# Kernel tuning notes

Measured on AMD Instinct MI355X. Metric: run time of the kernel, lower is better.

The kernel has to match this reference:

```python
import jax, jax.numpy as jnp
import numpy as np

N, F_IN, H, P, R = 50000, 384, 128, 128, 16
E = 500000


def _lin_params(key, fan_in, fan_out):
    k1, k2 = jax.random.split(key)
    s = 1.0 / np.sqrt(fan_in)
    W = jax.random.uniform(k1, (fan_in, fan_out), jnp.float32, -s, s)
    b = jax.random.uniform(k2, (fan_out,), jnp.float32, -s, s)
    return W, b


def setup_inputs() -> dict:
    key = jax.random.key(0)
    ks = jax.random.split(key, 16)
    x = jax.random.normal(ks[0], (N, F_IN), jnp.float32)
    edge_index = jax.random.randint(ks[1], (2, E), 0, N, jnp.int64)
    W_gcn1, b_gcn1 = _lin_params(ks[2], F_IN, H)
    W_ti, b_ti = _lin_params(ks[3], F_IN, F_IN)      # CrossFusion.text_info (384 -> dim=384)
    W_gi, b_gi = _lin_params(ks[4], H, F_IN)          # CrossFusion.graph_info (128 -> 384)
    W_v, b_v = _lin_params(ks[5], F_IN, F_IN)         # CrossFusion.value
    Wl1, bl1 = _lin_params(ks[6], F_IN, F_IN // 2)    # left_generator hidden
    Wl2, bl2 = _lin_params(ks[7], F_IN // 2, P * R)
    Wr1, br1 = _lin_params(ks[8], F_IN, F_IN // 2)    # right_generator hidden
    Wr2, br2 = _lin_params(ks[9], F_IN // 2, R * F_IN)
    W_gcn2, b_gcn2 = _lin_params(ks[10], P, H)        # fusion_gcn (128 -> 128)
    W_gp, b_gp = _lin_params(ks[11], P, P)            # graph_proj
    return dict(x=x, edge_index=edge_index, W_gcn1=W_gcn1, b_gcn1=b_gcn1,
                W_ti=W_ti, b_ti=b_ti, W_gi=W_gi, b_gi=b_gi, W_v=W_v, b_v=b_v,
                Wl1=Wl1, bl1=bl1, Wl2=Wl2, bl2=bl2, Wr1=Wr1, br1=br1, Wr2=Wr2, br2=br2,
                W_gcn2=W_gcn2, b_gcn2=b_gcn2, W_gp=W_gp, b_gp=b_gp)


def _gcn(x, W, b, src, dst, n):
    # PyG GCNConv: self-loops + symmetric degree normalization, aggregate at dst.
    xw = x @ W
    loop = jnp.arange(n, dtype=src.dtype)
    s = jnp.concatenate([src, loop])
    d = jnp.concatenate([dst, loop])
    deg = jax.ops.segment_sum(jnp.ones_like(d, dtype=xw.dtype), d, num_segments=n)
    dinv = jnp.where(deg > 0, jax.lax.rsqrt(deg), 0.0)
    norm = dinv[s] * dinv[d]                           # [E+N]
    out = jax.ops.segment_sum(norm[:, None] * xw[s], d, num_segments=n)
    return out + b


def _cross_fusion(text_feat, graph_feat, row, col, W_ti, b_ti, W_gi, b_gi, W_v, b_v):
    n, dim = text_feat.shape[0], W_ti.shape[1]
    t_info = text_feat @ W_ti + b_ti                   # [N, dim]
    g_info = graph_feat @ W_gi + b_gi                  # [N, dim]
    v = text_feat @ W_v + b_v                          # [N, dim]
    scores = jnp.sum(t_info[row] * g_info[col], axis=-1) / np.sqrt(dim)   # [E]
    m = jax.ops.segment_max(scores, row, num_segments=n)                  # scatter_softmax
    e = jnp.exp(scores - m[row])
    denom = jax.ops.segment_sum(e, row, num_segments=n)
    attn = e / denom[row]
    out = jax.ops.segment_sum(attn[:, None] * v[col], row, num_segments=n)
    return out + text_feat


def _forward(x, edge_index, W_gcn1, b_gcn1, W_ti, b_ti, W_gi, b_gi, W_v, b_v,
             Wl1, bl1, Wl2, bl2, Wr1, br1, Wr2, br2, W_gcn2, b_gcn2, W_gp, b_gp):
    src, dst = edge_index[0], edge_index[1]
    n = x.shape[0]
    g_emb = _gcn(x, W_gcn1, b_gcn1, src, dst, n)
    x_fused = _cross_fusion(x, g_emb, src, dst, W_ti, b_ti, W_gi, b_gi, W_v, b_v)
    # N > 40000 -> low-rank chunked projection (chunking is pure batching; vectorize)
    left = (jax.nn.relu(x_fused @ Wl1 + bl1) @ Wl2 + bl2).reshape(n, P, R)
    right = (jax.nn.relu(x_fused @ Wr1 + br1) @ Wr2 + br2).reshape(n, R, F_IN)
    temp = jnp.einsum('nrf,nf->nr', right, x)
    p_t = jnp.einsum('npr,nr->np', left, temp)         # [N, P]
    g2 = _gcn(p_t, W_gcn2, b_gcn2, src, dst, n)        # dropout is identity in eval
    p_g = g2 @ W_gp + b_gp
    p_t = p_t / jnp.maximum(jnp.linalg.norm(p_t, axis=-1, keepdims=True), 1e-12)
    p_g = p_g / jnp.maximum(jnp.linalg.norm(p_g, axis=-1, keepdims=True), 1e-12)
    alignment = jnp.sum(p_t * p_g, axis=1)
    return alignment, p_t, p_g, g2


def reference(x, edge_index, W_gcn1, b_gcn1, W_ti, b_ti, W_gi, b_gi, W_v, b_v,
              Wl1, bl1, Wl2, bl2, Wr1, br1, Wr2, br2, W_gcn2, b_gcn2, W_gp, b_gp):
    return _forward(x, edge_index, W_gcn1, b_gcn1, W_ti, b_ti, W_gi, b_gi, W_v, b_v,
                    Wl1, bl1, Wl2, bl2, Wr1, br1, Wr2, br2, W_gcn2, b_gcn2, W_gp, b_gp)
```

## Files before the change

kernel.cpp:

```cpp
#include <hip/hip_runtime.h>

typedef unsigned int u32;
typedef unsigned short u16;
typedef short s16x8 __attribute__((ext_vector_type(8)));
typedef u16 u16x8 __attribute__((ext_vector_type(8)));
typedef float f32x4 __attribute__((ext_vector_type(4)));

#define FIN 384
#define HD  128
#define PD  128
#define RD  16

#define GLOAD16(g, l)                                                          \
  __builtin_amdgcn_global_load_lds(                                            \
      (const __attribute__((address_space(1))) void*)(g),                      \
      (__attribute__((address_space(3))) void*)(l), 16, 0, 0)

__device__ __forceinline__ u16 f2bf(float f) {
  u32 u = __float_as_uint(f);
  u32 r = (u + 0x7fffu + ((u >> 16) & 1u)) >> 16;
  return (u16)r;
}
__device__ __forceinline__ float bf2f(u16 h) {
  return __uint_as_float(((u32)h) << 16);
}

__device__ __forceinline__ int xcd_wgid() {
  int nwg = gridDim.x, orig = blockIdx.x;
  int q = nwg >> 3, r = nwg & 7, xcd = orig & 7, idx = orig >> 3;
  return (xcd < r ? xcd * (q + 1) : r * (q + 1) + (xcd - r) * q) + idx;
}

struct CvtEnt { const float* s; u16* d; int K, N, mode, blk0; };
struct CvtDesc { CvtEnt e[12]; int n; };

__global__ void cvt_all_k(CvtDesc dsc) {
  int b = blockIdx.x;
  int ei = 0;
  while (ei + 1 < dsc.n && dsc.e[ei + 1].blk0 <= b) ++ei;
  CvtEnt E = dsc.e[ei];
  int i = (b - E.blk0) * 256 + (int)threadIdx.x;
  int tot = E.K * E.N;
  if (i >= tot) return;
  float v;
  if (E.mode == 0) {
    int c = i / E.K, k = i - c * E.K;
    v = E.s[(size_t)k * E.N + c];
  } else if (E.mode == 1) {
    v = E.s[i];
  } else {
    int q = i / 384, f = i - q * 384;
    v = E.s[(size_t)(q >> 4) * 6144 + (q & 15) * 384 + f];
  }
  E.d[i] = f2bf(v);
}

__global__ void hist_k(const int* __restrict__ src, const int* __restrict__ dst,
                       u32* __restrict__ cnt, int n, int E) {
  int i = blockIdx.x * 256 + threadIdx.x;
  if (i < E) {
    atomicAdd(&cnt[src[i]], 1u);
    atomicAdd(&cnt[n + dst[i]], 1u);
  }
}

__global__ __launch_bounds__(1024)
void scanA_k(const u32* __restrict__ cnt, u32* __restrict__ off,
             u32* __restrict__ bsum, int n2) {
  __shared__ u32 sh[1024];
  int i = blockIdx.x * 1024 + (int)threadIdx.x;
  u32 v = (i < n2) ? cnt[i] : 0u;
  sh[threadIdx.x] = v;
  __syncthreads();
  for (int s = 1; s < 1024; s <<= 1) {
    u32 t = (threadIdx.x >= (u32)s) ? sh[threadIdx.x - s] : 0u;
    __syncthreads();
    sh[threadIdx.x] += t;
    __syncthreads();
  }
  if (i < n2) off[i] = sh[threadIdx.x] - v;
  if (threadIdx.x == 1023) bsum[blockIdx.x] = sh[1023];
}

__global__ void scanB_k(u32* __restrict__ bsum, int nb) {
  int l = threadIdx.x;
  u32 carry = 0u;
  for (int base = 0; base < nb; base += 64) {
    u32 v = (base + l < nb) ? bsum[base + l] : 0u;
    for (int s = 1; s < 64; s <<= 1) {
      u32 t = __shfl_up(v, s);
      if (l >= s) v += t;
    }
    if (base + l < nb) bsum[base + l] = v + carry;
    carry += __shfl(v, 63);
  }
}

__global__ __launch_bounds__(1024)
void scanC_k(u32* __restrict__ off, u32* __restrict__ cur,
             const u32* __restrict__ bsum, int n2) {
  int b = blockIdx.x;
  int i = b * 1024 + (int)threadIdx.x;
  if (i >= n2) return;
  u32 add = (b > 0) ? bsum[b - 1] : 0u;
  u32 o = off[i] + add;
  off[i] = o;
  cur[i] = o;
}

__global__ void fill_k(const int* __restrict__ src, const int* __restrict__ dst,
                       u32* __restrict__ cur, u32* __restrict__ adj, int n, int E) {
  int i = blockIdx.x * 256 + threadIdx.x;
  if (i >= E) return;
  int s = src[i], d = dst[i];
  u32 ps = atomicAdd(&cur[s], 1u);
  adj[ps] = (u32)d;
  u32 pd = atomicAdd(&cur[n + d], 1u);
  adj[pd] = (u32)s;
}

__global__ void dinv_k(const u32* __restrict__ cd, float* __restrict__ dinv, int n) {
  int i = blockIdx.x * 256 + threadIdx.x;
  if (i < n) dinv[i] = 1.0f / sqrtf((float)(cd[i] + 1u));
}

template <int WF32, int WBF>
__global__ void gcn_agg_k(const u16* __restrict__ xw, const float* __restrict__ dinv,
                          const u32* __restrict__ off, const u32* __restrict__ cnt,
                          const u32* __restrict__ nbr, const float* __restrict__ bias,
                          float* __restrict__ outf, u16* __restrict__ outb, int n) {
  int node = (blockIdx.x * blockDim.x + threadIdx.x) >> 6;
  int lane = threadIdx.x & 63;
  if (node >= n) return;
  float di = dinv[node];
  ushort2 v = ((const ushort2*)(xw + (size_t)node * HD))[lane];
  float ax = di * di * bf2f(v.x), ay = di * di * bf2f(v.y);
  u32 i = off[node], end = i + cnt[node];
  for (; i + 4 <= end; i += 4) {
    int s0 = (int)nbr[i],     s1 = (int)nbr[i + 1];
    int s2 = (int)nbr[i + 2], s3 = (int)nbr[i + 3];
    float w0 = di * dinv[s0], w1 = di * dinv[s1];
    float w2 = di * dinv[s2], w3 = di * dinv[s3];
    ushort2 u0 = ((const ushort2*)(xw + (size_t)s0 * HD))[lane];
    ushort2 u1 = ((const ushort2*)(xw + (size_t)s1 * HD))[lane];
    ushort2 u2 = ((const ushort2*)(xw + (size_t)s2 * HD))[lane];
    ushort2 u3 = ((const ushort2*)(xw + (size_t)s3 * HD))[lane];
    ax = fmaf(w0, bf2f(u0.x), ax); ay = fmaf(w0, bf2f(u0.y), ay);
    ax = fmaf(w1, bf2f(u1.x), ax); ay = fmaf(w1, bf2f(u1.y), ay);
    ax = fmaf(w2, bf2f(u2.x), ax); ay = fmaf(w2, bf2f(u2.y), ay);
    ax = fmaf(w3, bf2f(u3.x), ax); ay = fmaf(w3, bf2f(u3.y), ay);
  }
  for (; i < end; ++i) {
    int s0 = (int)nbr[i];
    float w0 = di * dinv[s0];
    ushort2 u0 = ((const ushort2*)(xw + (size_t)s0 * HD))[lane];
    ax = fmaf(w0, bf2f(u0.x), ax);
    ay = fmaf(w0, bf2f(u0.y), ay);
  }
  float2 b = ((const float2*)bias)[lane];
  ax += b.x; ay += b.y;
  if (WF32) ((float2*)(outf + (size_t)node * HD))[lane] = make_float2(ax, ay);
  if (WBF) {
    ushort2 ob; ob.x = f2bf(ax); ob.y = f2bf(ay);
    ((ushort2*)(outb + (size_t)node * HD))[lane] = ob;
  }
}

__global__ void attn_fused_k(const u32* __restrict__ off, const u32* __restrict__ cnt,
                             const u32* __restrict__ adj,
                             const u16* __restrict__ ti, int TS,
                             const u16* __restrict__ gi, int GS,
                             const u16* __restrict__ vmat, int VS,
                             const u16* __restrict__ xb,
                             float* __restrict__ scores,
                             u16* __restrict__ xf, int n) {
  int node = (blockIdx.x * blockDim.x + threadIdx.x) >> 6;
  int lane = threadIdx.x & 63;
  if (node >= n) return;
  u32 o = off[node], c = cnt[node];
  u32 end = o + c;
  float acc[6] = {0.f, 0.f, 0.f, 0.f, 0.f, 0.f};
  const float sc = 0.05103103630798288f;
  if (c > 0) {
    const u16* tp = ti + (size_t)node * TS;
    float tf[6];
#pragma unroll
    for (int q = 0; q < 3; ++q) {
      ushort2 tv = *(const ushort2*)(tp + q * 128 + lane * 2);
      tf[q * 2] = bf2f(tv.x);
      tf[q * 2 + 1] = bf2f(tv.y);
    }
    if (c <= 64) {
      float sreg = -1e30f;
      u32 i = o;
      for (; i + 2 <= end; i += 2) {
        int d0 = (int)adj[i], d1 = (int)adj[i + 1];
        const u16* g0 = gi + (size_t)d0 * GS;
        const u16* g1 = gi + (size_t)d1 * GS;
        float dot0 = 0.f, dot1 = 0.f;
#pragma unroll
        for (int q = 0; q < 3; ++q) {
          ushort2 a = *(const ushort2*)(g0 + q * 128 + lane * 2);
          ushort2 b = *(const ushort2*)(g1 + q * 128 + lane * 2);
          dot0 = fmaf(tf[q * 2], bf2f(a.x), dot0);
          dot0 = fmaf(tf[q * 2 + 1], bf2f(a.y), dot0);
          dot1 = fmaf(tf[q * 2], bf2f(b.x), dot1);
          dot1 = fmaf(tf[q * 2 + 1], bf2f(b.y), dot1);
        }
#pragma unroll
        for (int s2 = 32; s2 >= 1; s2 >>= 1) {
          dot0 += __shfl_xor(dot0, s2);
          dot1 += __shfl_xor(dot1, s2);
        }
        int idx = (int)(i - o);
        if (lane == idx) sreg = dot0 * sc;
        if (lane == idx + 1) sreg = dot1 * sc;
      }
      if (i < end) {
        int d0 = (int)adj[i];
        const u16* g0 = gi + (size_t)d0 * GS;
        float dot0 = 0.f;
#pragma unroll
        for (int q = 0; q < 3; ++q) {
          ushort2 a = *(const ushort2*)(g0 + q * 128 + lane * 2);
          dot0 = fmaf(tf[q * 2], bf2f(a.x), dot0);
          dot0 = fmaf(tf[q * 2 + 1], bf2f(a.y), dot0);
        }
#pragma unroll
        for (int s2 = 32; s2 >= 1; s2 >>= 1) dot0 += __shfl_xor(dot0, s2);
        if (lane == (int)(i - o)) sreg = dot0 * sc;
      }
      float mx = sreg;
#pragma unroll
      for (int s2 = 32; s2 >= 1; s2 >>= 1) mx = fmaxf(mx, __shfl_xor(mx, s2));
      float ew = (lane < (int)c) ? expf(sreg - mx) : 0.f;
      float den = ew;
#pragma unroll
      for (int s2 = 32; s2 >= 1; s2 >>= 1) den += __shfl_xor(den, s2);
      float wreg = ew / den;
      i = o;
      for (; i + 2 <= end; i += 2) {
        int d0 = (int)adj[i], d1 = (int)adj[i + 1];
        int idx = (int)(i - o);
        float w0 = __shfl(wreg, idx);
        float w1 = __shfl(wreg, idx + 1);
        const u16* v0 = vmat + (size_t)d0 * VS;
        const u16* v1 = vmat + (size_t)d1 * VS;
#pragma unroll
        for (int q = 0; q < 3; ++q) {
          ushort2 a = *(const ushort2*)(v0 + q * 128 + lane * 2);
          ushort2 b = *(const ushort2*)(v1 + q * 128 + lane * 2);
          acc[q * 2]     = fmaf(w0, bf2f(a.x), acc[q * 2]);
          acc[q * 2 + 1] = fmaf(w0, bf2f(a.y), acc[q * 2 + 1]);
          acc[q * 2]     = fmaf(w1, bf2f(b.x), acc[q * 2]);
          acc[q * 2 + 1] = fmaf(w1, bf2f(b.y), acc[q * 2 + 1]);
        }
      }
      if (i < end) {
        int d0 = (int)adj[i];
        float w0 = __shfl(wreg, (int)(i - o));
        const u16* v0 = vmat + (size_t)d0 * VS;
#pragma unroll
        for (int q = 0; q < 3; ++q) {
          ushort2 a = *(const ushort2*)(v0 + q * 128 + lane * 2);
          acc[q * 2]     = fmaf(w0, bf2f(a.x), acc[q * 2]);
          acc[q * 2 + 1] = fmaf(w0, bf2f(a.y), acc[q * 2 + 1]);
        }
      }
    } else {
      float mx = -1e30f;
      u32 i = o;
      for (; i < end; ++i) {
        int d0 = (int)adj[i];
        const u16* g0 = gi + (size_t)d0 * GS;
        float dot0 = 0.f;
#pragma unroll
        for (int q = 0; q < 3; ++q) {
          ushort2 a = *(const ushort2*)(g0 + q * 128 + lane * 2);
          dot0 = fmaf(tf[q * 2], bf2f(a.x), dot0);
          dot0 = fmaf(tf[q * 2 + 1], bf2f(a.y), dot0);
        }
#pragma unroll
        for (int s2 = 32; s2 >= 1; s2 >>= 1) dot0 += __shfl_xor(dot0, s2);
        dot0 *= sc;
        if (lane == 0) scores[i] = dot0;
        mx = fmaxf(mx, dot0);
      }
      float den = 0.f;
      for (u32 k = o + lane; k < end; k += 64) den += expf(scores[k] - mx);
#pragma unroll
      for (int s2 = 32; s2 >= 1; s2 >>= 1) den += __shfl_xor(den, s2);
      float invden = 1.0f / den;
      for (i = o; i < end; ++i) {
        int d0 = (int)adj[i];
        float w0 = expf(scores[i] - mx) * invden;
        const u16* v0 = vmat + (size_t)d0 * VS;
#pragma unroll
        for (int q = 0; q < 3; ++q) {
          ushort2 a = *(const ushort2*)(v0 + q * 128 + lane * 2);
          acc[q * 2]     = fmaf(w0, bf2f(a.x), acc[q * 2]);
          acc[q * 2 + 1] = fmaf(w0, bf2f(a.y), acc[q * 2 + 1]);
        }
      }
    }
  }
  const u16* xp = xb + (size_t)node * FIN;
  u16* op = xf + (size_t)node * FIN;
#pragma unroll
  for (int q = 0; q < 3; ++q) {
    ushort2 xv = *(const ushort2*)(xp + q * 128 + lane * 2);
    ushort2 ov;
    ov.x = f2bf(acc[q * 2] + bf2f(xv.x));
    ov.y = f2bf(acc[q * 2 + 1] + bf2f(xv.y));
    *(ushort2*)(op + q * 128 + lane * 2) = ov;
  }
}

template <int EPI, int OUTBF>
__global__ __launch_bounds__(256)
void mgemm_k(const u16* __restrict__ Abf, int As, const u16* __restrict__ WT,
             const float* __restrict__ bias, const float* __restrict__ bias_b, int bsplit,
             void* __restrict__ Cp, u16* __restrict__ Cbf2,
             float* __restrict__ tmp, int M, int K, int Nc, int ncx) {
  __shared__ u16 Albuf[2][128 * 32];
  __shared__ u16 Blbuf[2][128 * 32];
  const int t = threadIdx.x;
  const int lane = t & 63;
  const int wave = t >> 6;
  const int wr = wave >> 1, wc = wave & 1;
  const int wgid = xcd_wgid();
  const int ctile = wgid % ncx;
  const int row0 = (wgid / ncx) * 128;
  const int col0 = ctile * 128;
  const int sr = t >> 2;
  const int sk = (t & 3) * 8;
  const int nt = K >> 5;

  f32x4 acc[4][4] = {};

  auto stage = [&](int buf, int k0) {
#pragma unroll
    for (int h = 0; h < 2; ++h) {
      int ar = row0 + h * 64 + sr;
      if (ar >= M) ar = M - 1;
      GLOAD16(Abf + (size_t)ar * As + k0 + sk, &Albuf[buf][h * 2048 + wave * 512]);
    }
#pragma unroll
    for (int h = 0; h < 2; ++h) {
      int bc = col0 + h * 64 + sr;
      if (bc >= Nc) bc = Nc - 1;
      GLOAD16(WT + (size_t)bc * K + k0 + sk, &Blbuf[buf][h * 2048 + wave * 512]);
    }
  };

  stage(0, 0);
  int buf = 0;
  for (int tk = 0; tk < nt; ++tk) {
    __syncthreads();
    if (tk + 1 < nt) stage(buf ^ 1, (tk + 1) << 5);
    const u16* Al = Albuf[buf];
    const u16* Bl = Blbuf[buf];
    s16x8 a[4], b[4];
#pragma unroll
    for (int m = 0; m < 4; ++m)
      a[m] = *(const s16x8*)(Al + (wr * 64 + m * 16 + (lane & 15)) * 32 + (lane >> 4) * 8);
#pragma unroll
    for (int j = 0; j < 4; ++j)
      b[j] = *(const s16x8*)(Bl + (wc * 64 + j * 16 + (lane & 15)) * 32 + (lane >> 4) * 8);
#pragma unroll
    for (int mc = 0; mc < 4; ++mc)
#pragma unroll
      for (int jr = 0; jr < 4; ++jr)
        acc[mc][jr] = __builtin_amdgcn_mfma_f32_16x16x32_bf16(b[mc], a[jr], acc[mc][jr], 0, 0, 0);
    buf ^= 1;
  }

  if constexpr (EPI <= 2) {
#pragma unroll
    for (int jr = 0; jr < 4; ++jr) {
      int row = row0 + wr * 64 + jr * 16 + (lane & 15);
      if (row >= M) continue;
#pragma unroll
      for (int mc = 0; mc < 4; ++mc) {
        int colb = col0 + wc * 64 + mc * 16 + (lane >> 4) * 4;
        if (colb >= Nc) continue;
        float4 bv = make_float4(0.f, 0.f, 0.f, 0.f);
        if (EPI >= 1) {
          const float* bp = (colb < bsplit) ? bias + colb : bias_b + (colb - bsplit);
          bv = *(const float4*)bp;
        }
        float v0 = acc[mc][jr][0] + bv.x;
        float v1 = acc[mc][jr][1] + bv.y;
        float v2 = acc[mc][jr][2] + bv.z;
        float v3 = acc[mc][jr][3] + bv.w;
        if (EPI == 2) {
          v0 = fmaxf(v0, 0.f); v1 = fmaxf(v1, 0.f);
          v2 = fmaxf(v2, 0.f); v3 = fmaxf(v3, 0.f);
        }
        if (OUTBF) {
          ushort4 ov;
          ov.x = f2bf(v0); ov.y = f2bf(v1); ov.z = f2bf(v2); ov.w = f2bf(v3);
          *(ushort4*)((u16*)Cp + (size_t)row * Nc + colb) = ov;
        } else {
          *(float4*)((float*)Cp + (size_t)row * Nc + colb) = make_float4(v0, v1, v2, v3);
        }
      }
    }
  } else if constexpr (EPI == 6) {
#pragma unroll
    for (int jr = 0; jr < 4; ++jr) {
      int row = row0 + wr * 64 + jr * 16 + (lane & 15);
      if (row >= M) continue;
#pragma unroll
      for (int mc = 0; mc < 4; ++mc) {
        int colb = col0 + wc * 64 + mc * 16 + (lane >> 4) * 4;
        if (colb < 2 * FIN) {
          const float* bp = (colb < bsplit) ? bias + colb : bias_b + (colb - bsplit);
          float4 bv = *(const float4*)bp;
          ushort4 ov;
          ov.x = f2bf(acc[mc][jr][0] + bv.x);
          ov.y = f2bf(acc[mc][jr][1] + bv.y);
          ov.z = f2bf(acc[mc][jr][2] + bv.z);
          ov.w = f2bf(acc[mc][jr][3] + bv.w);
          *(ushort4*)((u16*)Cp + (size_t)row * (2 * FIN) + colb) = ov;
        } else {
          int c2 = colb - 2 * FIN;
          ushort4 ov;
          ov.x = f2bf(acc[mc][jr][0]);
          ov.y = f2bf(acc[mc][jr][1]);
          ov.z = f2bf(acc[mc][jr][2]);
          ov.w = f2bf(acc[mc][jr][3]);
          *(ushort4*)(Cbf2 + (size_t)row * HD + c2) = ov;
        }
      }
    }
  } else {
    u16* slice = (u16*)Cp + (size_t)ctile * M * 8;
    float4 b4[4];
#pragma unroll
    for (int mc = 0; mc < 4; ++mc)
      b4[mc] = *(const float4*)&bias[col0 + wc * 64 + mc * 16 + (lane >> 4) * 4];
#pragma unroll
    for (int jr = 0; jr < 4; ++jr) {
      int row = row0 + wr * 64 + jr * 16 + (lane & 15);
      int rc = row < M ? row : M - 1;
      float4 tv = *(const float4*)&tmp[(size_t)rc * RD + (lane >> 4) * 4];
      ushort4 outp;
#pragma unroll
      for (int mc = 0; mc < 4; ++mc) {
        float s = (acc[mc][jr][0] + b4[mc].x) * tv.x +
                  (acc[mc][jr][1] + b4[mc].y) * tv.y +
                  (acc[mc][jr][2] + b4[mc].z) * tv.z +
                  (acc[mc][jr][3] + b4[mc].w) * tv.w;
        s += __shfl_xor(s, 16);
        s += __shfl_xor(s, 32);
        ((u16*)&outp)[mc] = f2bf(s);
      }
      if (lane < 16 && row < M)
        *(ushort4*)(slice + (size_t)row * 8 + wc * 4) = outp;
    }
  }
}

__global__ void ptgather_k(const u16* __restrict__ ptP, float* __restrict__ pt,
                           u16* __restrict__ ptb, int n) {
  int g = blockIdx.x * 256 + threadIdx.x;
  if (g >= n * 16) return;
  int row = g >> 4, ct = g & 15;
  const u16* sp = ptP + ((size_t)ct * n + (size_t)row) * 8;
  ushort4 a = ((const ushort4*)sp)[0];
  ushort4 b = ((const ushort4*)sp)[1];
  float* dp = pt + (size_t)row * PD + ct * 8;
  ((float4*)dp)[0] = make_float4(bf2f(a.x), bf2f(a.y), bf2f(a.z), bf2f(a.w));
  ((float4*)dp)[1] = make_float4(bf2f(b.x), bf2f(b.y), bf2f(b.z), bf2f(b.w));
  u16* db = ptb + (size_t)row * PD + ct * 8;
  ((ushort4*)db)[0] = a;
  ((ushort4*)db)[1] = b;
}

#define VM6  asm volatile("s_waitcnt vmcnt(6)" ::: "memory")
#define VM0  asm volatile("s_waitcnt vmcnt(0)" ::: "memory")
#define VMNOP
#define BARR asm volatile("s_barrier" ::: "memory")

__global__ __launch_bounds__(512)
void ygemm8_k(const u16* __restrict__ X, const u16* __restrict__ QT,
              const u16* __restrict__ Ar, float* __restrict__ tmpP, int M) {
  __shared__ u16 Al[2][16384];
  __shared__ u16 Bl[2][16384];
  const int t = threadIdx.x;
  const int lane = t & 63;
  const int wave = t >> 6;
  const int wr = wave >> 2;
  const int wcn = wave & 3;
  const int wgid = xcd_wgid();
  const int ctile = wgid % 12;
  const int row0 = (wgid / 12) * 256;
  const int col0 = ctile * 256;

  const int srow = t >> 3;
  const int sgk  = (((t & 7) ^ (srow & 7)) << 3);
  const int sdst = t * 8;

  const int pc0 = (((lane >> 4)) ^ (lane & 7)) << 3;
  const int pc1 = ((((lane >> 4) + 4)) ^ (lane & 7)) << 3;
  const int arow = (wr * 128 + (lane & 15)) << 6;
  const int brow = (wcn * 64 + (lane & 15)) << 6;

  f32x4 acc[8][4] = {};
  s16x8 a[4][2], b[4][2];

#define STGA8(bf, h, kt) do {                                                  \
    int r0_ = row0 + (h) * 128 + srow;                                         \
    int r1_ = r0_ + 64;                                                        \
    if (r0_ >= M) r0_ = M - 1;                                                 \
    if (r1_ >= M) r1_ = M - 1;                                                 \
    GLOAD16(X + (size_t)r0_ * 384 + (kt) * 64 + sgk, &Al[bf][(h) * 8192 + sdst]);        \
    GLOAD16(X + (size_t)r1_ * 384 + (kt) * 64 + sgk, &Al[bf][(h) * 8192 + 4096 + sdst]); \
  } while (0)

#define STGB8(bf, h, kt) do {                                                  \
    int c0_ = col0 + (h) * 128 + srow;                                         \
    GLOAD16(QT + (size_t)c0_ * 384 + (kt) * 64 + sgk, &Bl[bf][(h) * 8192 + sdst]);       \
    GLOAD16(QT + (size_t)(c0_ + 64) * 384 + (kt) * 64 + sgk,                   \
            &Bl[bf][(h) * 8192 + 4096 + sdst]);                                \
  } while (0)

#define LDA8(bf, mh) do {                                                      \
    _Pragma("unroll") for (int m2_ = 0; m2_ < 4; ++m2_) {                      \
      const u16* p_ = &Al[bf][arow + ((mh) * 4 + m2_) * 1024];                 \
      a[m2_][0] = *(const s16x8*)(p_ + pc0);                                   \
      a[m2_][1] = *(const s16x8*)(p_ + pc1);                                   \
    }                                                                          \
  } while (0)

#define LDB8(bf, jh) do {                                                      \
    _Pragma("unroll") for (int j2_ = 0; j2_ < 2; ++j2_) {                      \
      const u16* p_ = &Bl[bf][brow + ((jh) * 2 + j2_) * 1024];                 \
      b[(jh) * 2 + j2_][0] = *(const s16x8*)(p_ + pc0);                        \
      b[(jh) * 2 + j2_][1] = *(const s16x8*)(p_ + pc1);                        \
    }                                                                          \
  } while (0)

#define MQ8(mh, jh) do {                                                       \
    __builtin_amdgcn_s_setprio(1);                                             \
    _Pragma("unroll") for (int m2_ = 0; m2_ < 4; ++m2_)                        \
      _Pragma("unroll") for (int j2_ = 0; j2_ < 2; ++j2_)                      \
        _Pragma("unroll") for (int ks_ = 0; ks_ < 2; ++ks_)                    \
          acc[(mh) * 4 + m2_][(jh) * 2 + j2_] =                                \
              __builtin_amdgcn_mfma_f32_16x16x32_bf16(                         \
                  a[m2_][ks_], b[(jh) * 2 + j2_][ks_],                         \
                  acc[(mh) * 4 + m2_][(jh) * 2 + j2_], 0, 0, 0);               \
    __builtin_amdgcn_s_setprio(0);                                             \
  } while (0)

  STGA8(0, 0, 0); STGA8(0, 1, 0); STGB8(0, 0, 0); STGB8(0, 1, 0);
  STGA8(1, 0, 1); STGB8(1, 0, 1); STGB8(1, 1, 1);
  VM6; BARR;

#define ITER8(i, VMP3, VMP7, DOSTG)                                                          \
   LDA8(0,0); LDB8(0,0); STGA8(1,1,2*(i)+1);                   BARR; MQ8(0,0); BARR;  \
   LDB8(0,1);                                                  BARR; MQ8(0,1); BARR;  \
   LDA8(0,1); if (DOSTG) STGB8(0,0,2*(i)+2);                   BARR; MQ8(1,0); BARR;  \
   if (DOSTG) { STGB8(0,1,2*(i)+2); STGA8(0,0,2*(i)+2); } VMP3; BARR; MQ8(1,1); BARR; \
   LDA8(1,0); LDB8(1,0); if (DOSTG) STGA8(0,1,2*(i)+2);        BARR; MQ8(0,0); BARR;  \
   LDB8(1,1);                                                  BARR; MQ8(0,1); BARR;  \
   LDA8(1,1); if (DOSTG) STGB8(1,0,2*(i)+3);                   BARR; MQ8(1,0); BARR;  \
   if (DOSTG) { STGB8(1,1,2*(i)+3); STGA8(1,0,2*(i)+3); } VMP7; BARR; MQ8(1,1); BARR;

  ITER8(0, VM6, VM6, 1)
  ITER8(1, VM6, VM6, 1)
  ITER8(2, VM0, VMNOP, 0)

  const int h0 = (col0 >> 4) + wcn * 4;
  float s[8][4];
#pragma unroll
  for (int m = 0; m < 8; ++m) {
#pragma unroll
    for (int rr = 0; rr < 4; ++rr) {
      int row = row0 + wr * 128 + m * 16 + (lane >> 4) * 4 + rr;
      int rc = row < M ? row : M - 1;
      ushort4 arv = *(const ushort4*)(Ar + (size_t)rc * 384 + h0);
      s[m][rr] = bf2f(arv.x) * acc[m][0][rr] + bf2f(arv.y) * acc[m][1][rr] +
                 bf2f(arv.z) * acc[m][2][rr] + bf2f(arv.w) * acc[m][3][rr];
    }
  }

  __syncthreads();
  float* redA = (float*)&Al[0][0];
  float* redB = redA + 4096;
  const int r16 = lane & 15;
  const int rlb = wr * 128 + (lane >> 4) * 4;
  if (wcn & 1) {
    float* red = (wcn == 1) ? redA : redB;
#pragma unroll
    for (int m = 0; m < 8; ++m)
#pragma unroll
      for (int rr = 0; rr < 4; ++rr)
        red[(rlb + m * 16 + rr) * 16 + r16] = s[m][rr];
  }
  __syncthreads();
  if (!(wcn & 1)) {
    float* red = (wcn == 0) ? redA : redB;
#pragma unroll
    for (int m = 0; m < 8; ++m)
#pragma unroll
      for (int rr = 0; rr < 4; ++rr)
        s[m][rr] += red[(rlb + m * 16 + rr) * 16 + r16];
  }
  __syncthreads();
  if (wcn == 2) {
#pragma unroll
    for (int m = 0; m < 8; ++m)
#pragma unroll
      for (int rr = 0; rr < 4; ++rr)
        redA[(rlb + m * 16 + rr) * 16 + r16] = s[m][rr];
  }
  __syncthreads();
  if (wcn == 0) {
    float* slice = tmpP + (size_t)ctile * M * RD;
#pragma unroll
    for (int m = 0; m < 8; ++m)
#pragma unroll
      for (int rr = 0; rr < 4; ++rr) {
        int row = row0 + rlb + m * 16 + rr;
        if (row < M)
          slice[(size_t)row * RD + r16] =
              s[m][rr] + redA[(rlb + m * 16 + rr) * 16 + r16];
      }
  }
#undef STGA8
#undef STGB8
#undef LDA8
#undef LDB8
#undef MQ8
#undef ITER8
}

__global__ void combine_k(const float* __restrict__ tmpP, float* __restrict__ temp,
                          size_t sl, int tot4) {
  int i = blockIdx.x * 256 + threadIdx.x;
  if (i >= tot4) return;
  float4 s = ((const float4*)(tmpP + 12 * sl))[i];
#pragma unroll
  for (int c = 0; c < 12; ++c) {
    float4 p = ((const float4*)(tmpP + (size_t)c * sl))[i];
    s.x += p.x; s.y += p.y; s.z += p.z; s.w += p.w;
  }
  ((float4*)temp)[i] = s;
}

__global__ void final_k(float* __restrict__ out, int n) {
  int node = (blockIdx.x * blockDim.x + threadIdx.x) >> 6;
  int lane = threadIdx.x & 63;
  if (node >= n) return;
  float* pt = out + n + (size_t)node * PD;
  float* pg = out + n + (size_t)n * PD + (size_t)node * PD;
  float2 t = ((float2*)pt)[lane];
  float2 g = ((float2*)pg)[lane];
  float tt = t.x * t.x + t.y * t.y;
  float gg = g.x * g.x + g.y * g.y;
  float tg = t.x * g.x + t.y * g.y;
#pragma unroll
  for (int s = 32; s >= 1; s >>= 1) {
    tt += __shfl_xor(tt, s);
    gg += __shfl_xor(gg, s);
    tg += __shfl_xor(tg, s);
  }
  float invt = 1.0f / fmaxf(sqrtf(tt), 1e-12f);
  float invg = 1.0f / fmaxf(sqrtf(gg), 1e-12f);
  ((float2*)pt)[lane] = make_float2(t.x * invt, t.y * invt);
  ((float2*)pg)[lane] = make_float2(g.x * invg, g.y * invg);
  if (lane == 0) out[node] = tg * invt * invg;
}

struct MgArgs {
  const u16* A; int As; const u16* WT;
  const float* b; const float* b2; int bsplit;
  void* C; u16* C2; float* tmp;
  int M, K, Nc;
};
template <int EPI, int OUTBF>
static void mg(const MgArgs& a, hipStream_t s) {
  int ncx = (a.Nc + 127) / 128, nry = (a.M + 127) / 128;
  mgemm_k<EPI, OUTBF><<<dim3(ncx * nry), 256, 0, s>>>(
      a.A, a.As, a.WT, a.b, a.b2, a.bsplit, a.C, a.C2, a.tmp,
      a.M, a.K, a.Nc, ncx);
}

extern "C" void kernel_launch(void* const* d_in, const int* in_sizes, int n_in,
                              void* d_out, int out_size, void* d_ws, size_t ws_size,
                              hipStream_t stream) {
  const float* x      = (const float*)d_in[0];
  const int*   ei     = (const int*)d_in[1];
  const float* W_gcn1 = (const float*)d_in[2];
  const float* b_gcn1 = (const float*)d_in[3];
  const float* W_ti   = (const float*)d_in[4];
  const float* b_ti   = (const float*)d_in[5];
  const float* W_gi   = (const float*)d_in[6];
  const float* b_gi   = (const float*)d_in[7];
  const float* W_v    = (const float*)d_in[8];
  const float* b_v    = (const float*)d_in[9];
  const float* Wl1    = (const float*)d_in[10];
  const float* bl1    = (const float*)d_in[11];
  const float* Wl2    = (const float*)d_in[12];
  const float* bl2    = (const float*)d_in[13];
  const float* Wr1    = (const float*)d_in[14];
  const float* br1    = (const float*)d_in[15];
  const float* Wr2    = (const float*)d_in[16];
  const float* br2    = (const float*)d_in[17];
  const float* W_gcn2 = (const float*)d_in[18];
  const float* b_gcn2 = (const float*)d_in[19];
  const float* W_gp   = (const float*)d_in[20];
  const float* b_gp   = (const float*)d_in[21];

  const int n = in_sizes[0] / FIN;
  const int E = in_sizes[1] / 2;
  const int* src = ei;
  const int* dst = ei + E;

  char* wsp = (char*)d_ws;
  auto carve = [&](size_t bytes) -> void* {
    void* p = (void*)wsp;
    wsp += (bytes + 255) & ~(size_t)255;
    return p;
  };
  u32* cnt      = (u32*)carve((size_t)2 * n * 4);
  u32* off      = (u32*)carve((size_t)2 * n * 4);
  u32* cur      = (u32*)carve((size_t)2 * n * 4);
  u32* bsum     = (u32*)carve(512);
  u32* adj      = (u32*)carve((size_t)2 * E * 4);
  float* dinv   = (float*)carve((size_t)n * 4);
  float* scores = (float*)carve((size_t)E * 4);
  float* temp   = (float*)carve((size_t)n * RD * 4);

  u16* xbf    = (u16*)carve((size_t)n * FIN * 2);
  u16* tvbf   = (u16*)carve((size_t)n * 2 * FIN * 2);
  u16* bufHbf = (u16*)carve((size_t)n * HD * 2);
  u16* gembf  = (u16*)carve((size_t)n * HD * 2);
  u16* ptbf   = (u16*)carve((size_t)n * PD * 2);
  u16* g2bf   = (u16*)carve((size_t)n * HD * 2);

  u16* gibf   = (u16*)carve((size_t)n * FIN * 2);
  u16* xfbf   = (u16*)carve((size_t)n * FIN * 2);
  size_t tmpP_bytes = (size_t)13 * n * RD * 4;
  size_t overlay    = (size_t)2 * n * FIN * 2;
  carve(tmpP_bytes > overlay ? tmpP_bytes - overlay : 0);
  float* tmpP = (float*)gibf;
  u16* ptP    = (u16*)gibf;

  u16* WtvT   = (u16*)carve((size_t)2 * FIN * FIN * 2);
  u16* WgcnT  = (u16*)carve((size_t)HD * FIN * 2);
  u16* WgiT   = (u16*)carve((size_t)FIN * HD * 2);
  u16* WlrT   = (u16*)carve((size_t)FIN * FIN * 2);
  u16* Wl2T   = (u16*)carve((size_t)2048 * 192 * 2);
  u16* QT     = (u16*)carve((size_t)3072 * FIN * 2);
  u16* BrT    = (u16*)carve((size_t)RD * FIN * 2);
  u16* Wgcn2T = (u16*)carve((size_t)HD * PD * 2);
  u16* WgpT   = (u16*)carve((size_t)PD * PD * 2);

  u16* lrbf = tvbf;

  float* out    = (float*)d_out;
  float* pt_raw = out + n;
  float* pg_raw = out + n + (size_t)n * PD;
  float* g2     = out + n + (size_t)2 * n * PD;

  CvtDesc dsc;
  int nent = 0, blk = 0;
  auto addent = [&](const float* s, u16* d, int K, int N, int mode) {
    dsc.e[nent] = {s, d, K, N, mode, blk};
    blk += (K * N + 255) / 256;
    ++nent;
  };
  addent(x,      xbf,    n * FIN, 1, 1);
  addent(W_ti,   WtvT,   FIN, FIN, 0);
  addent(W_v,    WtvT + (size_t)FIN * FIN, FIN, FIN, 0);
  addent(W_gcn1, WgcnT,  FIN, HD,  0);
  addent(W_gi,   WgiT,   HD,  FIN, 0);
  addent(Wl1,    WlrT,   FIN, 192, 0);
  addent(Wr1,    WlrT + (size_t)192 * FIN, FIN, 192, 0);
  addent(Wl2,    Wl2T,   192, 2048, 0);
  addent(Wr2,    QT,     FIN, 3072, 2);
  addent(br2,    BrT,    RD * FIN, 1, 1);
  addent(W_gcn2, Wgcn2T, PD, HD, 0);
  addent(W_gp,   WgpT,   PD, PD, 0);
  dsc.n = nent;
  cvt_all_k<<<blk, 256, 0, stream>>>(dsc);

  hipMemsetAsync(cnt, 0, (size_t)2 * n * 4, stream);
  hist_k<<<(E + 255) / 256, 256, 0, stream>>>(src, dst, cnt, n, E);
  int n2 = 2 * n;
  int nb = (n2 + 1023) / 1024;
  scanA_k<<<nb, 1024, 0, stream>>>(cnt, off, bsum, n2);
  scanB_k<<<1, 64, 0, stream>>>(bsum, nb);
  scanC_k<<<nb, 1024, 0, stream>>>(off, cur, bsum, n2);
  fill_k<<<(E + 255) / 256, 256, 0, stream>>>(src, dst, cur, adj, n, E);
  dinv_k<<<(n + 255) / 256, 256, 0, stream>>>(cnt + n, dinv, n);

  MgArgs a{};

  a = {xbf, FIN, WtvT, b_ti, b_v, FIN, tvbf, bufHbf, nullptr, n, FIN, 896};
  mg<6, 1>(a, stream);
  gcn_agg_k<0, 1><<<(n + 3) / 4, 256, 0, stream>>>(bufHbf, dinv, off + n, cnt + n, adj,
                                                   b_gcn1, nullptr, gembf, n);

  a = {gembf, HD, WgiT, b_gi, nullptr, 1 << 30, gibf, nullptr, nullptr, n, HD, FIN};
  mg<1, 1>(a, stream);
  attn_fused_k<<<(n + 3) / 4, 256, 0, stream>>>(off, cnt, adj, tvbf, 2 * FIN, gibf, FIN,
                                                tvbf + FIN, 2 * FIN, xbf, scores, xfbf, n);

  a = {xfbf, FIN, WlrT, bl1, br1, 192, lrbf, nullptr, nullptr, n, FIN, FIN};
  mg<2, 1>(a, stream);

  a = {xbf, FIN, BrT, nullptr, nullptr, 1 << 30, tmpP + (size_t)12 * n * RD, nullptr,
       nullptr, n, FIN, RD};
  mg<0, 0>(a, stream);
  ygemm8_k<<<dim3(12 * ((n + 255) / 256)), 512, 0, stream>>>(xbf, QT, lrbf + 192,
                                                             tmpP, n);
  combine_k<<<(n * RD / 4 + 255) / 256, 256, 0, stream>>>(tmpP, temp, (size_t)n * RD,
                                                          n * RD / 4);

  a = {lrbf, FIN, Wl2T, bl2, nullptr, 1 << 30, ptP, nullptr, temp, n, 192, PD * RD};
  mg<4, 0>(a, stream);
  ptgather_k<<<(n * 16 + 255) / 256, 256, 0, stream>>>(ptP, pt_raw, ptbf, n);

  a = {ptbf, PD, Wgcn2T, nullptr, nullptr, 1 << 30, bufHbf, nullptr, nullptr, n, PD, HD};
  mg<0, 1>(a, stream);
  gcn_agg_k<1, 1><<<(n + 3) / 4, 256, 0, stream>>>(bufHbf, dinv, off + n, cnt + n, adj,
                                                   b_gcn2, g2, g2bf, n);
  a = {g2bf, HD, WgpT, b_gp, nullptr, 1 << 30, pg_raw, nullptr, nullptr, n, HD, PD};
  mg<1, 0>(a, stream);

  final_k<<<(n + 3) / 4, 256, 0, stream>>>(out, n);
}
```

Baseline: 789.6 us.

## Use single-pass online softmax in cross-fusion attention kernel

Replaces the two-pass attention (scores first, then softmax-weighted value gather) with one pass that keeps a running max and denominator, as in flash attention. Each neighbor's key row and value row are loaded together, so the adjacency list is walked once and the separate high-degree path with its global scores buffer is gone. The cost is two extra exps per edge and a rescale of the accumulators at every step.

```diff
diff --git a/kernel.cpp b/kernel.cpp
--- a/kernel.cpp
+++ b/kernel.cpp
@@ -172,7 +172,6 @@
                              const u16* __restrict__ gi, int GS,
                              const u16* __restrict__ vmat, int VS,
                              const u16* __restrict__ xb,
-                             float* __restrict__ scores,
                              u16* __restrict__ xf, int n) {
   int node = (blockIdx.x * blockDim.x + threadIdx.x) >> 6;
   int lane = threadIdx.x & 63;
@@ -190,119 +189,94 @@
       tf[q * 2] = bf2f(tv.x);
       tf[q * 2 + 1] = bf2f(tv.y);
     }
-    if (c <= 64) {
-      float sreg = -1e30f;
-      u32 i = o;
-      for (; i + 2 <= end; i += 2) {
-        int d0 = (int)adj[i], d1 = (int)adj[i + 1];
-        const u16* g0 = gi + (size_t)d0 * GS;
-        const u16* g1 = gi + (size_t)d1 * GS;
-        float dot0 = 0.f, dot1 = 0.f;
+    float m = -1e30f, den = 0.f;
+    u32 i = o;
+    for (; i + 2 <= end; i += 2) {
+      int d0 = (int)adj[i], d1 = (int)adj[i + 1];
+      const u16* g0 = gi + (size_t)d0 * GS;
+      const u16* g1 = gi + (size_t)d1 * GS;
+      const u16* v0 = vmat + (size_t)d0 * VS;
+      const u16* v1 = vmat + (size_t)d1 * VS;
+      ushort2 ga[3], gb[3], va[3], vb[3];
+#pragma unroll
+      for (int q = 0; q < 3; ++q) {
+        ga[q] = *(const ushort2*)(g0 + q * 128 + lane * 2);
+        gb[q] = *(const ushort2*)(g1 + q * 128 + lane * 2);
+        va[q] = *(const ushort2*)(v0 + q * 128 + lane * 2);
+        vb[q] = *(const ushort2*)(v1 + q * 128 + lane * 2);
+      }
+      float dot0 = 0.f, dot1 = 0.f;
+#pragma unroll
+      for (int q = 0; q < 3; ++q) {
+        dot0 = fmaf(tf[q * 2], bf2f(ga[q].x), dot0);
+        dot0 = fmaf(tf[q * 2 + 1], bf2f(ga[q].y), dot0);
+        dot1 = fmaf(tf[q * 2], bf2f(gb[q].x), dot1);
+        dot1 = fmaf(tf[q * 2 + 1], bf2f(gb[q].y), dot1);
+      }
+#pragma unroll
+      for (int s2 = 32; s2 >= 1; s2 >>= 1) {
+        dot0 += __shfl_xor(dot0, s2);
+        dot1 += __shfl_xor(dot1, s2);
+      }
+      dot0 *= sc; dot1 *= sc;
+      {
+        float m1 = fmaxf(m, dot0);
+        float sc0 = expf(m - m1);
+        float e0 = expf(dot0 - m1);
+        den = den * sc0 + e0;
 #pragma unroll
         for (int q = 0; q < 3; ++q) {
-          ushort2 a = *(const ushort2*)(g0 + q * 128 + lane * 2);
-          ushort2 b = *(const ushort2*)(g1 + q * 128 + lane * 2);
-          dot0 = fmaf(tf[q * 2], bf2f(a.x), dot0);
-          dot0 = fmaf(tf[q * 2 + 1], bf2f(a.y), dot0);
-          dot1 = fmaf(tf[q * 2], bf2f(b.x), dot1);
-          dot1 = fmaf(tf[q * 2 + 1], bf2f(b.y), dot1);
+          acc[q * 2]     = acc[q * 2]     * sc0 + e0 * bf2f(va[q].x);
+          acc[q * 2 + 1] = acc[q * 2 + 1] * sc0 + e0 * bf2f(va[q].y);
         }
-#pragma unroll
-        for (int s2 = 32; s2 >= 1; s2 >>= 1) {
-          dot0 += __shfl_xor(dot0, s2);
-          dot1 += __shfl_xor(dot1, s2);
+        m = m1;
+      }
+      {
+        float m1 = fmaxf(m, dot1);
+        float sc1 = expf(m - m1);
+        float e1 = expf(dot1 - m1);
+        den = den * sc1 + e1;
+#pragma unroll
+        for (int q = 0; q < 3; ++q) {
+          acc[q * 2]     = acc[q * 2]     * sc1 + e1 * bf2f(vb[q].x);
+          acc[q * 2 + 1] = acc[q * 2 + 1] * sc1 + e1 * bf2f(vb[q].y);
         }
-        int idx = (int)(i - o);
-        if (lane == idx) sreg = dot0 * sc;
-        if (lane == idx + 1) sreg = dot1 * sc;
-      }
-      if (i < end) {
-        int d0 = (int)adj[i];
-        const u16* g0 = gi + (size_t)d0 * GS;
-        float dot0 = 0.f;
-#pragma unroll
-        for (int q = 0; q < 3; ++q) {
-          ushort2 a = *(const ushort2*)(g0 + q * 128 + lane * 2);
-          dot0 = fmaf(tf[q * 2], bf2f(a.x), dot0);
-          dot0 = fmaf(tf[q * 2 + 1], bf2f(a.y), dot0);
-        }
-#pragma unroll
-        for (int s2 = 32; s2 >= 1; s2 >>= 1) dot0 += __shfl_xor(dot0, s2);
-        if (lane == (int)(i - o)) sreg = dot0 * sc;
-      }
-      float mx = sreg;
-#pragma unroll
-      for (int s2 = 32; s2 >= 1; s2 >>= 1) mx = fmaxf(mx, __shfl_xor(mx, s2));
-      float ew = (lane < (int)c) ? expf(sreg - mx) : 0.f;
-      float den = ew;
-#pragma unroll
-      for (int s2 = 32; s2 >= 1; s2 >>= 1) den += __shfl_xor(den, s2);
-      float wreg = ew / den;
-      i = o;
-      for (; i + 2 <= end; i += 2) {
-        int d0 = (int)adj[i], d1 = (int)adj[i + 1];
-        int idx = (int)(i - o);
-        float w0 = __shfl(wreg, idx);
-        float w1 = __shfl(wreg, idx + 1);
-        const u16* v0 = vmat + (size_t)d0 * VS;
-        const u16* v1 = vmat + (size_t)d1 * VS;
-#pragma unroll
-        for (int q = 0; q < 3; ++q) {
-          ushort2 a = *(const ushort2*)(v0 + q * 128 + lane * 2);
-          ushort2 b = *(const ushort2*)(v1 + q * 128 + lane * 2);
-          acc[q * 2]     = fmaf(w0, bf2f(a.x), acc[q * 2]);
-          acc[q * 2 + 1] = fmaf(w0, bf2f(a.y), acc[q * 2 + 1]);
-          acc[q * 2]     = fmaf(w1, bf2f(b.x), acc[q * 2]);
-          acc[q * 2 + 1] = fmaf(w1, bf2f(b.y), acc[q * 2 + 1]);
-        }
-      }
-      if (i < end) {
-        int d0 = (int)adj[i];
-        float w0 = __shfl(wreg, (int)(i - o));
-        const u16* v0 = vmat + (size_t)d0 * VS;
-#pragma unroll
-        for (int q = 0; q < 3; ++q) {
-          ushort2 a = *(const ushort2*)(v0 + q * 128 + lane * 2);
-          acc[q * 2]     = fmaf(w0, bf2f(a.x), acc[q * 2]);
-          acc[q * 2 + 1] = fmaf(w0, bf2f(a.y), acc[q * 2 + 1]);
-        }
-      }
-    } else {
-      float mx = -1e30f;
-      u32 i = o;
-      for (; i < end; ++i) {
-        int d0 = (int)adj[i];
-        const u16* g0 = gi + (size_t)d0 * GS;
-        float dot0 = 0.f;
-#pragma unroll
-        for (int q = 0; q < 3; ++q) {
-          ushort2 a = *(const ushort2*)(g0 + q * 128 + lane * 2);
-          dot0 = fmaf(tf[q * 2], bf2f(a.x), dot0);
-          dot0 = fmaf(tf[q * 2 + 1], bf2f(a.y), dot0);
-        }
-#pragma unroll
-        for (int s2 = 32; s2 >= 1; s2 >>= 1) dot0 += __shfl_xor(dot0, s2);
-        dot0 *= sc;
-        if (lane == 0) scores[i] = dot0;
-        mx = fmaxf(mx, dot0);
-      }
-      float den = 0.f;
-      for (u32 k = o + lane; k < end; k += 64) den += expf(scores[k] - mx);
-#pragma unroll
-      for (int s2 = 32; s2 >= 1; s2 >>= 1) den += __shfl_xor(den, s2);
-      float invden = 1.0f / den;
-      for (i = o; i < end; ++i) {
-        int d0 = (int)adj[i];
-        float w0 = expf(scores[i] - mx) * invden;
-        const u16* v0 = vmat + (size_t)d0 * VS;
-#pragma unroll
-        for (int q = 0; q < 3; ++q) {
-          ushort2 a = *(const ushort2*)(v0 + q * 128 + lane * 2);
-          acc[q * 2]     = fmaf(w0, bf2f(a.x), acc[q * 2]);
-          acc[q * 2 + 1] = fmaf(w0, bf2f(a.y), acc[q * 2 + 1]);
-        }
-      }
-    }
+        m = m1;
+      }
+    }
+    if (i < end) {
+      int d0 = (int)adj[i];
+      const u16* g0 = gi + (size_t)d0 * GS;
+      const u16* v0 = vmat + (size_t)d0 * VS;
+      ushort2 ga[3], va[3];
+#pragma unroll
+      for (int q = 0; q < 3; ++q) {
+        ga[q] = *(const ushort2*)(g0 + q * 128 + lane * 2);
+        va[q] = *(const ushort2*)(v0 + q * 128 + lane * 2);
+      }
+      float dot0 = 0.f;
+#pragma unroll
+      for (int q = 0; q < 3; ++q) {
+        dot0 = fmaf(tf[q * 2], bf2f(ga[q].x), dot0);
+        dot0 = fmaf(tf[q * 2 + 1], bf2f(ga[q].y), dot0);
+      }
+#pragma unroll
+      for (int s2 = 32; s2 >= 1; s2 >>= 1) dot0 += __shfl_xor(dot0, s2);
+      dot0 *= sc;
+      float m1 = fmaxf(m, dot0);
+      float sc0 = expf(m - m1);
+      float e0 = expf(dot0 - m1);
+      den = den * sc0 + e0;
+#pragma unroll
+      for (int q = 0; q < 3; ++q) {
+        acc[q * 2]     = acc[q * 2]     * sc0 + e0 * bf2f(va[q].x);
+        acc[q * 2 + 1] = acc[q * 2 + 1] * sc0 + e0 * bf2f(va[q].y);
+      }
+      m = m1;
+    }
+    float invden = 1.0f / den;
+#pragma unroll
+    for (int k = 0; k < 6; ++k) acc[k] *= invden;
   }
   const u16* xp = xb + (size_t)node * FIN;
   u16* op = xf + (size_t)node * FIN;
@@ -731,7 +705,6 @@
   u32* bsum     = (u32*)carve(512);
   u32* adj      = (u32*)carve((size_t)2 * E * 4);
   float* dinv   = (float*)carve((size_t)n * 4);
-  float* scores = (float*)carve((size_t)E * 4);
   float* temp   = (float*)carve((size_t)n * RD * 4);
 
   u16* xbf    = (u16*)carve((size_t)n * FIN * 2);
@@ -808,7 +781,7 @@
   a = {gembf, HD, WgiT, b_gi, nullptr, 1 << 30, gibf, nullptr, nullptr, n, HD, FIN};
   mg<1, 1>(a, stream);
   attn_fused_k<<<(n + 3) / 4, 256, 0, stream>>>(off, cnt, adj, tvbf, 2 * FIN, gibf, FIN,
-                                                tvbf + FIN, 2 * FIN, xbf, scores, xfbf, n);
+                                                tvbf + FIN, 2 * FIN, xbf, xfbf, n);
 
   a = {xfbf, FIN, WlrT, bl1, br1, 192, lrbf, nullptr, nullptr, n, FIN, FIN};
   mg<2, 1>(a, stream);
```

After: 784.8 us. No clear change (-0.6%).
